# Optimization experiments

Hardware: AMD Instinct MI355X
Metric: run time of the kernel (lower is better)

## Reference

```python
import jax, jax.numpy as jnp
import numpy as np


def setup_inputs() -> dict:
    key = jax.random.key(0)
    ks = jax.random.split(key, 8)
    B, C, H, W = 4, 128, 128, 128
    C8 = C // 8
    x = jax.random.normal(ks[0], (B, C, H, W), jnp.float32)
    # 1x1 conv weights as [out, in] matrices + biases
    Wq = jax.random.normal(ks[1], (C8, C), jnp.float32) * 0.05
    bq = jax.random.normal(ks[2], (C8,), jnp.float32) * 0.01
    Wk = jax.random.normal(ks[3], (C8, C), jnp.float32) * 0.05
    bk = jax.random.normal(ks[4], (C8,), jnp.float32) * 0.01
    Wv = jax.random.normal(ks[5], (C, C), jnp.float32) * 0.05
    bv = jax.random.normal(ks[6], (C,), jnp.float32) * 0.01
    # nn.Parameter(torch.zeros(1)) in the original; use nonzero so output/grads are nontrivial
    gamma = jax.random.normal(ks[7], (), jnp.float32) * 0.1
    return {"x": x, "Wq": Wq, "bq": bq, "Wk": Wk, "bk": bk,
            "Wv": Wv, "bv": bv, "gamma": gamma}


def reference(x, Wq, bq, Wk, bk, Wv, bv, gamma):
    # x: [b, c, h, w]
    b, c, h, w = x.shape
    # 1x1 convs == channel contractions
    q = jnp.einsum('bchw,oc->bohw', x, Wq) + bq[None, :, None, None]  # [b,c8,h,w]
    k = jnp.einsum('bchw,oc->bohw', x, Wk) + bk[None, :, None, None]  # [b,c8,h,w]
    v = jnp.einsum('bchw,oc->bohw', x, Wv) + bv[None, :, None, None]  # [b,c, h,w]

    # column (height) attention logits: e_h[b, h1, w, h2], diagonal masked to -inf
    e_h = jnp.einsum('bcxw,bcyw->bxwy', q, k)
    diag = jnp.eye(h, dtype=bool)  # [h1, h2]
    e_h = jnp.where(diag[:, None, :], -jnp.inf, e_h)
    # row (width) attention logits: e_w[b, h, w1, w2]
    e_w = jnp.einsum('bchx,bchy->bhxy', q, k)

    # joint softmax over concatenated (h2 + w2) axis
    attn = jax.nn.softmax(jnp.concatenate([e_h, e_w], axis=3), axis=3)  # [b,h,w,h+w]
    attn_h = attn[..., :h]   # [b, h1, w, h2]
    attn_w = attn[..., h:]   # [b, h, w1, w2]

    # aggregate values along columns and rows
    out_h = jnp.einsum('bcyw,bxwy->bcxw', v, attn_h)  # [b,c,h,w]
    out_w = jnp.einsum('bchy,bhxy->bchx', v, attn_w)  # [b,c,h,w]

    out = gamma * (out_h + out_w) + x
    # return_attn: stack([b h2 h1 w, b w2 h w1], dim=1)
    return_attn = jnp.stack([jnp.transpose(attn_h, (0, 3, 1, 2)),
                             jnp.transpose(attn_w, (0, 3, 1, 2))], axis=1)
    return out, return_attn
```

## Files before the change

kernel.cpp:

```cpp
#include <hip/hip_runtime.h>
#include <math.h>

#define HW_ 16384
#define SLOT_ 2097152ULL
#define BSTR_ 4194304ULL

typedef __attribute__((ext_vector_type(8))) short short8v;
typedef __attribute__((ext_vector_type(4))) float f32x4;

__device__ __forceinline__ unsigned short f2bf(float f) {
  unsigned int u = __float_as_uint(f);
  u = (u + 0x7FFFu + ((u >> 16) & 1u)) >> 16;
  return (unsigned short)u;
}
__device__ __forceinline__ float bf2f(unsigned short h) {
  return __uint_as_float(((unsigned int)h) << 16);
}

__global__ void __launch_bounds__(512, 4)
qkv_proj(const float* __restrict__ x,
         const float* __restrict__ Wq, const float* __restrict__ bq,
         const float* __restrict__ Wk, const float* __restrict__ bk,
         const float* __restrict__ Wv, const float* __restrict__ bv,
         float* __restrict__ qT, float* __restrict__ kT,
         unsigned short* __restrict__ vA0,
         unsigned short* __restrict__ Ew, float* __restrict__ rsw) {
  __shared__ float WT[128][36];
  __shared__ float BUF[8448];
  float (*Wc)[132] = (float(*)[132])BUF;
  float (*Xc)[132] = (float(*)[132])(BUF + 4224);
  int t = threadIdx.x;
  for (int i = t; i < 4096; i += 512) {
    int o = i >> 7, c = i & 127;
    WT[c][o] = (o < 16) ? Wq[o * 128 + c] : Wk[(o - 16) * 128 + c];
  }
  int blk = blockIdx.x;
  int b = blk >> 7, h = blk & 127;
  int p0 = h * 128;
  int cg = t & 31;
  int pg = t >> 5;
  float acc[4][8];
#pragma unroll
  for (int ci = 0; ci < 4; ++ci) {
    float bvv = bv[cg * 4 + ci];
#pragma unroll
    for (int pi = 0; pi < 8; ++pi) acc[ci][pi] = bvv;
  }
  float accqk[8];
  {
    float bias = (cg < 16) ? bq[cg] : bk[cg - 16];
#pragma unroll
    for (int pi = 0; pi < 8; ++pi) accqk[pi] = bias;
  }
  int c2 = t >> 2, part = t & 3;
  const float* xb = x + (size_t)b * 128 * HW_ + p0;
  float4 pw[2], px[2];
#pragma unroll
  for (int q = 0; q < 2; ++q)
    pw[q] = *(const float4*)&Wv[c2 * 128 + part * 8 + q * 4];
#pragma unroll
  for (int r = 0; r < 2; ++r) {
    int idx = r * 2048 + t * 4;
    px[r] = *(const float4*)&xb[(size_t)(idx >> 7) * HW_ + (idx & 127)];
  }
  __syncthreads();
  for (int k0 = 0; k0 < 128; k0 += 32) {
#pragma unroll
    for (int q = 0; q < 2; ++q) {
      int y4 = part * 8 + q * 4;
      Wc[y4 + 0][c2] = pw[q].x;
      Wc[y4 + 1][c2] = pw[q].y;
      Wc[y4 + 2][c2] = pw[q].z;
      Wc[y4 + 3][c2] = pw[q].w;
    }
#pragma unroll
    for (int r = 0; r < 2; ++r) {
      int idx = r * 2048 + t * 4;
      *(float4*)&Xc[idx >> 7][idx & 127] = px[r];
    }
    __syncthreads();
    if (k0 < 96) {
#pragma unroll
      for (int q = 0; q < 2; ++q)
        pw[q] = *(const float4*)&Wv[c2 * 128 + (k0 + 32) + part * 8 + q * 4];
#pragma unroll
      for (int r = 0; r < 2; ++r) {
        int idx = r * 2048 + t * 4;
        px[r] = *(const float4*)&xb[(size_t)(k0 + 32 + (idx >> 7)) * HW_ + (idx & 127)];
      }
    }
    for (int kl = 0; kl < 32; ++kl) {
      float wa[4], xa[8];
      *(float4*)(wa)     = *(const float4*)&Wc[kl][cg * 4];
      *(float4*)(xa)     = *(const float4*)&Xc[kl][pg * 8];
      *(float4*)(xa + 4) = *(const float4*)&Xc[kl][pg * 8 + 4];
      float wq = WT[k0 + kl][cg];
#pragma unroll
      for (int ci = 0; ci < 4; ++ci)
#pragma unroll
        for (int pi = 0; pi < 8; ++pi)
          acc[ci][pi] = fmaf(wa[ci], xa[pi], acc[ci][pi]);
#pragma unroll
      for (int pi = 0; pi < 8; ++pi)
        accqk[pi] = fmaf(wq, xa[pi], accqk[pi]);
    }
    __syncthreads();
  }
#pragma unroll
  for (int ci = 0; ci < 4; ++ci) {
    union { unsigned short us[8]; uint4 v; } pk;
#pragma unroll
    for (int pi = 0; pi < 8; ++pi) pk.us[pi] = f2bf(acc[ci][pi]);
    *(uint4*)&vA0[(size_t)(b * 128 + h) * 16384 + (size_t)(cg * 4 + ci) * 128 + pg * 8] = pk.v;
  }
  float (*QKs)[36] = (float(*)[36])BUF;
#pragma unroll
  for (int pi = 0; pi < 8; ++pi)
    QKs[pg * 8 + pi][cg] = accqk[pi];
  __syncthreads();
  if (t >= 256) {
    int tt = t - 256;
    int px_ = tt >> 1, sel = tt & 1;
    const float* qr = &QKs[px_][sel * 16];
    float4 r0 = *(const float4*)(qr);
    float4 r1 = *(const float4*)(qr + 4);
    float4 r2 = *(const float4*)(qr + 8);
    float4 r3 = *(const float4*)(qr + 12);
    float* dstT = (sel ? kT : qT) + ((size_t)(b * HW_ + px_ * 128 + h)) * 16;
    *(float4*)(dstT)      = r0;
    *(float4*)(dstT + 4)  = r1;
    *(float4*)(dstT + 8)  = r2;
    *(float4*)(dstT + 12) = r3;
  } else {
    float (*Qs)[132] = (float(*)[132])&WT[0][0];
    float (*Ks)[132] = (float(*)[132])(&WT[0][0] + 2112);
    int cc = t & 15, pb = (t >> 4) * 8;
#pragma unroll
    for (int u = 0; u < 8; ++u) {
      Qs[cc][pb + u] = QKs[pb + u][cc];
      Ks[cc][pb + u] = QKs[pb + u][16 + cc];
    }
  }
  __syncthreads();
  if (t < 256) {
    float (*Qs)[132] = (float(*)[132])&WT[0][0];
    float (*Ks)[132] = (float(*)[132])(&WT[0][0] + 2112);
    int tr = (t >> 4) * 8;
    int ty = (t & 15) * 8;
    float sc_[8][8] = {{0.f}};
#pragma unroll
    for (int c = 0; c < 16; ++c) {
      float qa[8], ka[8];
      *(float4*)(qa)     = *(const float4*)&Qs[c][tr];
      *(float4*)(qa + 4) = *(const float4*)&Qs[c][tr + 4];
      *(float4*)(ka)     = *(const float4*)&Ks[c][ty];
      *(float4*)(ka + 4) = *(const float4*)&Ks[c][ty + 4];
#pragma unroll
      for (int u = 0; u < 8; ++u)
#pragma unroll
        for (int v = 0; v < 8; ++v)
          sc_[u][v] = fmaf(qa[u], ka[v], sc_[u][v]);
    }
    float rp[8];
#pragma unroll
    for (int u = 0; u < 8; ++u) {
      rp[u] = 0.f;
#pragma unroll
      for (int v = 0; v < 8; ++v) {
        float e = __expf(sc_[u][v]);
        sc_[u][v] = e;
        rp[u] += e;
      }
    }
    unsigned short* out = Ew + (size_t)blk * 16384;
#pragma unroll
    for (int u = 0; u < 8; ++u) {
      union { unsigned short us[8]; uint4 v; } pk;
#pragma unroll
      for (int v = 0; v < 8; ++v) pk.us[v] = f2bf(sc_[u][v]);
      *(uint4*)&out[(tr + u) * 128 + ty] = pk.v;
    }
#pragma unroll
    for (int u = 0; u < 8; ++u) {
      rp[u] += __shfl_xor(rp[u], 1);
      rp[u] += __shfl_xor(rp[u], 2);
      rp[u] += __shfl_xor(rp[u], 4);
      rp[u] += __shfl_xor(rp[u], 8);
    }
    if ((t & 15) == 0) {
#pragma unroll
      for (int u = 0; u < 8; ++u) rsw[(size_t)blk * 128 + tr + u] = rp[u];
    }
  }
}

__global__ void score_h(const float* __restrict__ Q, const float* __restrict__ K,
                        unsigned short* __restrict__ E, float* __restrict__ rsum,
                        size_t ebs, size_t eoff) {
  __shared__ float Qs[16][132];
  __shared__ float Ks[16][132];
  int slab = blockIdx.x;
  int b = slab >> 7, s = slab & 127;
  const float* qb = Q + (size_t)slab * 2048;
  const float* kb = K + (size_t)slab * 2048;
  int t = threadIdx.x;
  int cc = t & 15;
  int pb = (t >> 4) * 8;
#pragma unroll
  for (int u = 0; u < 8; ++u) {
    Qs[cc][pb + u] = qb[(size_t)(pb + u) * 16 + cc];
    Ks[cc][pb + u] = kb[(size_t)(pb + u) * 16 + cc];
  }
  __syncthreads();
  int tr = (t >> 4) * 8;
  int ty = (t & 15) * 8;
  float acc[8][8] = {{0.f}};
#pragma unroll
  for (int c = 0; c < 16; ++c) {
    float qa[8], ka[8];
    *(float4*)(qa)     = *(const float4*)&Qs[c][tr];
    *(float4*)(qa + 4) = *(const float4*)&Qs[c][tr + 4];
    *(float4*)(ka)     = *(const float4*)&Ks[c][ty];
    *(float4*)(ka + 4) = *(const float4*)&Ks[c][ty + 4];
#pragma unroll
    for (int u = 0; u < 8; ++u)
#pragma unroll
      for (int v = 0; v < 8; ++v)
        acc[u][v] = fmaf(qa[u], ka[v], acc[u][v]);
  }
  float rp[8];
#pragma unroll
  for (int u = 0; u < 8; ++u) {
    rp[u] = 0.f;
#pragma unroll
    for (int v = 0; v < 8; ++v) {
      float e = __expf(acc[u][v]);
      if ((tr + u) == (ty + v)) e = 0.f;
      acc[u][v] = e;
      rp[u] += e;
    }
  }
  unsigned short* out = E + (size_t)b * ebs + eoff + (size_t)s * 16384;
#pragma unroll
  for (int u = 0; u < 8; ++u) {
    union { unsigned short us[8]; uint4 v; } pk;
#pragma unroll
    for (int v = 0; v < 8; ++v) pk.us[v] = f2bf(acc[u][v]);
    *(uint4*)&out[(tr + u) * 128 + ty] = pk.v;
  }
#pragma unroll
  for (int u = 0; u < 8; ++u) {
    rp[u] += __shfl_xor(rp[u], 1);
    rp[u] += __shfl_xor(rp[u], 2);
    rp[u] += __shfl_xor(rp[u], 4);
    rp[u] += __shfl_xor(rp[u], 8);
  }
  if ((t & 15) == 0) {
#pragma unroll
    for (int u = 0; u < 8; ++u) rsum[(size_t)slab * 128 + tr + u] = rp[u];
  }
}

__global__ void trans_v(const unsigned short* __restrict__ vA0, unsigned short* __restrict__ vA1,
                        const float* __restrict__ rsw, const float* __restrict__ rsh,
                        float* __restrict__ dij, float* __restrict__ dji) {
  __shared__ unsigned short tile[64][65];
  int blk = blockIdx.x;
  int q = blk & 3, c = (blk >> 2) & 127, b = blk >> 9;
  int h0 = (q >> 1) * 64, w0 = (q & 1) * 64;
  int t = threadIdx.x, lane = t & 63, r0 = (t >> 6) * 16;
  for (int r = r0; r < r0 + 16; ++r)
    tile[r][lane] = vA0[(size_t)(b * 128 + h0 + r) * 16384 + c * 128 + w0 + lane];
  __syncthreads();
  for (int r = r0; r < r0 + 16; ++r)
    vA1[(size_t)(b * 128 + w0 + r) * 16384 + c * 128 + h0 + lane] = tile[lane][r];
  if (blk < 256) {
    int p = blk * 256 + t;
    int bb = p >> 14, rem = p & 16383, i = rem >> 7, j = rem & 127;
    float d = rsw[p] + rsh[(size_t)bb * HW_ + j * 128 + i];
    float r = 1.0f / d;
    dij[p] = r;
    dji[(size_t)bb * HW_ + j * 128 + i] = r;
  }
}

__global__ void pv2(const unsigned short* __restrict__ vA0,
                    const unsigned short* __restrict__ vA1,
                    const unsigned short* __restrict__ Ew,
                    const unsigned short* __restrict__ EhB,
                    const float* __restrict__ dij, const float* __restrict__ dji,
                    unsigned short* __restrict__ ow, unsigned short* __restrict__ ohb) {
  __shared__ unsigned short Al[128][44];
  __shared__ unsigned short Bl[128][44];
  int blk = blockIdx.x;
  int m = blk >> 9;
  int slab = blk & 511;
  int s = slab & 127, b = slab >> 7;
  int t = threadIdx.x;
  int wv = t >> 6, l = t & 63;
  int wc = (wv >> 1) * 64, wx = (wv & 1) * 64;
  const unsigned short* vs = (m ? vA1 : vA0) + (size_t)slab * 16384;
  const unsigned short* es = m ? (EhB + (size_t)b * 8388608 + 4194304 + (size_t)s * 16384)
                               : (Ew + (size_t)slab * 16384);
  const float* invd = m ? dji : dij;
  f32x4 acc[4][4];
#pragma unroll
  for (int mi = 0; mi < 4; ++mi)
#pragma unroll
    for (int ni = 0; ni < 4; ++ni) acc[mi][ni] = (f32x4){0.f, 0.f, 0.f, 0.f};
  int lrow = t >> 2, lq = t & 3;
  int lm = l & 15, lk = (l >> 4) * 4;
  for (int y0 = 0; y0 < 128; y0 += 32) {
#pragma unroll
    for (int r = 0; r < 2; ++r) {
      int rr = lrow + r * 64;
      uint4 av = *(const uint4*)(vs + (size_t)rr * 128 + y0 + lq * 8);
      uint4 bv = *(const uint4*)(es + (size_t)rr * 128 + y0 + lq * 8);
      *(uint2*)&Al[rr][lq * 8]     = make_uint2(av.x, av.y);
      *(uint2*)&Al[rr][lq * 8 + 4] = make_uint2(av.z, av.w);
      *(uint2*)&Bl[rr][lq * 8]     = make_uint2(bv.x, bv.y);
      *(uint2*)&Bl[rr][lq * 8 + 4] = make_uint2(bv.z, bv.w);
    }
    __syncthreads();
    short8v af[4], bf[4];
#pragma unroll
    for (int mi = 0; mi < 4; ++mi) {
      const unsigned short* ap = &Al[wc + mi * 16 + lm][lk];
      union { uint2 p[2]; short8v v; } u;
      u.p[0] = *(const uint2*)ap;
      u.p[1] = *(const uint2*)(ap + 16);
      af[mi] = u.v;
    }
#pragma unroll
    for (int ni = 0; ni < 4; ++ni) {
      const unsigned short* bp = &Bl[wx + ni * 16 + lm][lk];
      union { uint2 p[2]; short8v v; } u;
      u.p[0] = *(const uint2*)bp;
      u.p[1] = *(const uint2*)(bp + 16);
      bf[ni] = u.v;
    }
#pragma unroll
    for (int mi = 0; mi < 4; ++mi)
#pragma unroll
      for (int ni = 0; ni < 4; ++ni)
        acc[mi][ni] = __builtin_amdgcn_mfma_f32_16x16x32_bf16(af[mi], bf[ni], acc[mi][ni], 0, 0, 0);
    __syncthreads();
  }
  int lr4 = (l >> 4) * 4;
  unsigned short* dst = m ? ohb : ow;
#pragma unroll
  for (int ni = 0; ni < 4; ++ni) {
    int xx = wx + ni * 16 + lm;
    float idv = invd[(size_t)(b * 128 + s) * 128 + xx];
#pragma unroll
    for (int mi = 0; mi < 4; ++mi) {
#pragma unroll
      for (int r = 0; r < 4; ++r) {
        int c = wc + mi * 16 + lr4 + r;
        size_t idx = m ? ((size_t)b * 8388608 + (size_t)s * 16384 + (size_t)c * 128 + xx)
                       : ((((size_t)(b * 128 + c)) * 128 + s) * 128 + xx);
        dst[idx] = f2bf(acc[mi][ni][r] * idv);
      }
    }
  }
}

__global__ void merge2(const unsigned short* __restrict__ ow,
                       const unsigned short* __restrict__ ohp,
                       const float* __restrict__ xin, const float* __restrict__ gamma,
                       float* __restrict__ outp) {
  __shared__ float tile[64][65];
  int blk = blockIdx.x;
  int q = blk & 3, c = (blk >> 2) & 127, b = blk >> 9;
  int h0 = (q >> 1) * 64, w0 = (q & 1) * 64;
  int t = threadIdx.x, lane = t & 63, r0 = (t >> 6) * 16;
  for (int r = r0; r < r0 + 16; ++r)
    tile[r][lane] =
        bf2f(ohp[(size_t)b * 8388608ULL + (size_t)(w0 + r) * 16384 + c * 128 + h0 + lane]);
  __syncthreads();
  float g = gamma[0];
  for (int r = r0; r < r0 + 16; ++r) {
    size_t a = (((size_t)(b * 128 + c)) * 128 + h0 + r) * 128 + w0 + lane;
    outp[a] = g * (bf2f(ow[a]) + tile[lane][r]) + xin[a];
  }
}

template <int HM>
__global__ void ret_write(const unsigned short* __restrict__ src, const float* __restrict__ invd,
                          float* __restrict__ retb, size_t sbs, size_t soff) {
  __shared__ float tile[128][129];
  __shared__ float idv[128];
  int slab = blockIdx.x;
  int b = slab >> 7, i = slab & 127;
  int t = threadIdx.x;
  const unsigned short* sp = src + (size_t)b * sbs + soff;
#pragma unroll
  for (int r = 0; r < 8; ++r) {
    int idx = r * 2048 + t * 8;
    int j = idx >> 7, y = idx & 127;
    uint4 raw;
    if (HM == 0)
      raw = *(const uint4*)(sp + (size_t)i * 16384 + j * 128 + y);
    else
      raw = *(const uint4*)(sp + (size_t)j * 16384 + i * 128 + y);
    unsigned int wd[4] = {raw.x, raw.y, raw.z, raw.w};
#pragma unroll
    for (int e = 0; e < 4; ++e) {
      tile[j][y + 2 * e]     = __uint_as_float((wd[e] & 0xFFFFu) << 16);
      tile[j][y + 2 * e + 1] = __uint_as_float(wd[e] & 0xFFFF0000u);
    }
  }
  if (t < 128) idv[t] = invd[(size_t)slab * 128 + t];
  __syncthreads();
  float* dp = retb + (size_t)b * BSTR_ + (HM == 0 ? SLOT_ : 0);
#pragma unroll
  for (int r = 0; r < 16; ++r) {
    int idx = r * 1024 + t * 4;
    int y = idx >> 7, j = idx & 127;
    float4 o;
    o.x = tile[j][y]     * idv[j];
    o.y = tile[j + 1][y] * idv[j + 1];
    o.z = tile[j + 2][y] * idv[j + 2];
    o.w = tile[j + 3][y] * idv[j + 3];
    *(float4*)&dp[(size_t)y * 16384 + i * 128 + j] = o;
  }
}

extern "C" void kernel_launch(void* const* d_in, const int* in_sizes, int n_in,
                              void* d_out, int out_size, void* d_ws, size_t ws_size,
                              hipStream_t stream) {
  const float* x     = (const float*)d_in[0];
  const float* Wq    = (const float*)d_in[1];
  const float* bq    = (const float*)d_in[2];
  const float* Wk    = (const float*)d_in[3];
  const float* bk    = (const float*)d_in[4];
  const float* Wv    = (const float*)d_in[5];
  const float* bv    = (const float*)d_in[6];
  const float* gamma = (const float*)d_in[7];

  float* outp = (float*)d_out;
  float* retb = outp + (size_t)8388608;
  unsigned short* ohb = (unsigned short*)retb;
  unsigned short* ehb = (unsigned short*)retb;

  float* ws      = (float*)d_ws;
  float* qT      = ws + (size_t)2097152;
  float* kT      = ws + (size_t)3145728;
  unsigned short* ow  = (unsigned short*)ws;
  unsigned short* vA0 = (unsigned short*)(ws + (size_t)4194304);
  unsigned short* vA1 = (unsigned short*)(ws + (size_t)8388608);
  unsigned short* E_w = (unsigned short*)(ws + (size_t)12582912);
  float* rsum_w  = ws + (size_t)16777216;
  float* rsum_h  = ws + (size_t)16842752;
  float* invd_ij = ws + (size_t)16908288;
  float* invd_ji = ws + (size_t)16973824;

  qkv_proj<<<512, 512, 0, stream>>>(x, Wq, bq, Wk, bk, Wv, bv,
                                    qT, kT, vA0, E_w, rsum_w);
  score_h<<<512, 256, 0, stream>>>(qT, kT, ehb, rsum_h,
                                   (size_t)8388608, (size_t)4194304);
  trans_v<<<2048, 256, 0, stream>>>(vA0, vA1, rsum_w, rsum_h, invd_ij, invd_ji);
  pv2<<<1024, 256, 0, stream>>>(vA0, vA1, E_w, ehb, invd_ij, invd_ji, ow, ohb);
  merge2<<<2048, 256, 0, stream>>>(ow, ohb, x, gamma, outp);
  ret_write<1><<<512, 256, 0, stream>>>(ehb, invd_ij, retb, (size_t)8388608, (size_t)4194304);
  ret_write<0><<<512, 256, 0, stream>>>(E_w, invd_ij, retb, (size_t)2097152, (size_t)0);
}
```

Before: 139.5 us.

## Load full x and Wv tiles into LDS once instead of double-buffered k-chunks

The qkv projection kernel no longer streams x and Wv in four 32-wide k-chunks through registers with a sync per chunk. It now loads the whole 128x128 x tile and the transposed Wv into a single ~150KB LDS buffer up front, then runs one 128-step k loop with no intermediate barriers. This removes per-chunk barriers and register staging, but uses far more LDS, which cuts occupancy (launch bounds lowered to 2 blocks) and loses the overlap of global loads with compute.

```diff
diff --git a/kernel.cpp b/kernel.cpp
--- a/kernel.cpp
+++ b/kernel.cpp
@@ -17,7 +17,7 @@
   return __uint_as_float(((unsigned int)h) << 16);
 }
 
-__global__ void __launch_bounds__(512, 4)
+__global__ void __launch_bounds__(512, 2)
 qkv_proj(const float* __restrict__ x,
          const float* __restrict__ Wq, const float* __restrict__ bq,
          const float* __restrict__ Wk, const float* __restrict__ bk,
@@ -25,18 +25,37 @@
          float* __restrict__ qT, float* __restrict__ kT,
          unsigned short* __restrict__ vA0,
          unsigned short* __restrict__ Ew, float* __restrict__ rsw) {
-  __shared__ float WT[128][36];
-  __shared__ float BUF[8448];
-  float (*Wc)[132] = (float(*)[132])BUF;
-  float (*Xc)[132] = (float(*)[132])(BUF + 4224);
+  __shared__ float LDS[38400];
+  float (*XL)[132]  = (float(*)[132])LDS;
+  float (*WL)[132]  = (float(*)[132])(LDS + 16896);
+  float (*WTL)[36]  = (float(*)[36])(LDS + 33792);
   int t = threadIdx.x;
-  for (int i = t; i < 4096; i += 512) {
-    int o = i >> 7, c = i & 127;
-    WT[c][o] = (o < 16) ? Wq[o * 128 + c] : Wk[(o - 16) * 128 + c];
-  }
   int blk = blockIdx.x;
   int b = blk >> 7, h = blk & 127;
   int p0 = h * 128;
+  const float* xb = x + (size_t)b * 128 * HW_ + p0;
+  for (int i = t; i < 4096; i += 512) {
+    int o = i >> 7, c = i & 127;
+    WTL[c][o] = (o < 16) ? Wq[o * 128 + c] : Wk[(o - 16) * 128 + c];
+  }
+#pragma unroll
+  for (int it = 0; it < 8; ++it) {
+    int gi = it * 512 + t;
+    int c = gi >> 5;
+    int p4 = (gi & 31) * 4;
+    *(float4*)&XL[c][p4] = *(const float4*)&xb[(size_t)c * HW_ + p4];
+  }
+#pragma unroll
+  for (int it = 0; it < 8; ++it) {
+    int gi = it * 512 + t;
+    int ch = gi >> 5;
+    int k4 = (gi & 31) * 4;
+    float4 w = *(const float4*)&Wv[ch * 128 + k4];
+    WL[k4 + 0][ch] = w.x;
+    WL[k4 + 1][ch] = w.y;
+    WL[k4 + 2][ch] = w.z;
+    WL[k4 + 3][ch] = w.w;
+  }
   int cg = t & 31;
   int pg = t >> 5;
   float acc[4][8];
@@ -52,59 +71,22 @@
 #pragma unroll
     for (int pi = 0; pi < 8; ++pi) accqk[pi] = bias;
   }
-  int c2 = t >> 2, part = t & 3;
-  const float* xb = x + (size_t)b * 128 * HW_ + p0;
-  float4 pw[2], px[2];
-#pragma unroll
-  for (int q = 0; q < 2; ++q)
-    pw[q] = *(const float4*)&Wv[c2 * 128 + part * 8 + q * 4];
-#pragma unroll
-  for (int r = 0; r < 2; ++r) {
-    int idx = r * 2048 + t * 4;
-    px[r] = *(const float4*)&xb[(size_t)(idx >> 7) * HW_ + (idx & 127)];
-  }
-  __syncthreads();
-  for (int k0 = 0; k0 < 128; k0 += 32) {
-#pragma unroll
-    for (int q = 0; q < 2; ++q) {
-      int y4 = part * 8 + q * 4;
-      Wc[y4 + 0][c2] = pw[q].x;
-      Wc[y4 + 1][c2] = pw[q].y;
-      Wc[y4 + 2][c2] = pw[q].z;
-      Wc[y4 + 3][c2] = pw[q].w;
-    }
-#pragma unroll
-    for (int r = 0; r < 2; ++r) {
-      int idx = r * 2048 + t * 4;
-      *(float4*)&Xc[idx >> 7][idx & 127] = px[r];
-    }
-    __syncthreads();
-    if (k0 < 96) {
-#pragma unroll
-      for (int q = 0; q < 2; ++q)
-        pw[q] = *(const float4*)&Wv[c2 * 128 + (k0 + 32) + part * 8 + q * 4];
-#pragma unroll
-      for (int r = 0; r < 2; ++r) {
-        int idx = r * 2048 + t * 4;
-        px[r] = *(const float4*)&xb[(size_t)(k0 + 32 + (idx >> 7)) * HW_ + (idx & 127)];
-      }
-    }
-    for (int kl = 0; kl < 32; ++kl) {
-      float wa[4], xa[8];
-      *(float4*)(wa)     = *(const float4*)&Wc[kl][cg * 4];
-      *(float4*)(xa)     = *(const float4*)&Xc[kl][pg * 8];
-      *(float4*)(xa + 4) = *(const float4*)&Xc[kl][pg * 8 + 4];
-      float wq = WT[k0 + kl][cg];
-#pragma unroll
-      for (int ci = 0; ci < 4; ++ci)
-#pragma unroll
-        for (int pi = 0; pi < 8; ++pi)
-          acc[ci][pi] = fmaf(wa[ci], xa[pi], acc[ci][pi]);
+  __syncthreads();
+#pragma unroll 4
+  for (int kl = 0; kl < 128; ++kl) {
+    float wa[4], xa[8];
+    *(float4*)(wa)     = *(const float4*)&WL[kl][cg * 4];
+    *(float4*)(xa)     = *(const float4*)&XL[kl][pg * 8];
+    *(float4*)(xa + 4) = *(const float4*)&XL[kl][pg * 8 + 4];
+    float wq = WTL[kl][cg];
+#pragma unroll
+    for (int ci = 0; ci < 4; ++ci)
 #pragma unroll
       for (int pi = 0; pi < 8; ++pi)
-        accqk[pi] = fmaf(wq, xa[pi], accqk[pi]);
-    }
-    __syncthreads();
+        acc[ci][pi] = fmaf(wa[ci], xa[pi], acc[ci][pi]);
+#pragma unroll
+    for (int pi = 0; pi < 8; ++pi)
+      accqk[pi] = fmaf(wq, xa[pi], accqk[pi]);
   }
 #pragma unroll
   for (int ci = 0; ci < 4; ++ci) {
@@ -113,7 +95,8 @@
     for (int pi = 0; pi < 8; ++pi) pk.us[pi] = f2bf(acc[ci][pi]);
     *(uint4*)&vA0[(size_t)(b * 128 + h) * 16384 + (size_t)(cg * 4 + ci) * 128 + pg * 8] = pk.v;
   }
-  float (*QKs)[36] = (float(*)[36])BUF;
+  __syncthreads();
+  float (*QKs)[36] = (float(*)[36])LDS;
 #pragma unroll
   for (int pi = 0; pi < 8; ++pi)
     QKs[pg * 8 + pi][cg] = accqk[pi];
@@ -132,8 +115,8 @@
     *(float4*)(dstT + 8)  = r2;
     *(float4*)(dstT + 12) = r3;
   } else {
-    float (*Qs)[132] = (float(*)[132])&WT[0][0];
-    float (*Ks)[132] = (float(*)[132])(&WT[0][0] + 2112);
+    float (*Qs)[132] = (float(*)[132])(LDS + 16896);
+    float (*Ks)[132] = (float(*)[132])(LDS + 16896 + 2112);
     int cc = t & 15, pb = (t >> 4) * 8;
 #pragma unroll
     for (int u = 0; u < 8; ++u) {
@@ -143,8 +126,8 @@
   }
   __syncthreads();
   if (t < 256) {
-    float (*Qs)[132] = (float(*)[132])&WT[0][0];
-    float (*Ks)[132] = (float(*)[132])(&WT[0][0] + 2112);
+    float (*Qs)[132] = (float(*)[132])(LDS + 16896);
+    float (*Ks)[132] = (float(*)[132])(LDS + 16896 + 2112);
     int tr = (t >> 4) * 8;
     int ty = (t & 15) * 8;
     float sc_[8][8] = {{0.f}};
```

Measured after the change: 143.0 us. 1.02x slower.
